# Performance work log

Measured on AMD Instinct MI355X. Metric: run time of the kernel, lower is better.

## Reference

```python
import jax, jax.numpy as jnp
import numpy as np

EPS = 1e-5
QSCALE = 2.0 ** 7  # input bitwidth 8 -> deterministic quantize round(x*2^(b-1))/2^(b-1)

@jax.custom_vjp
def ste_sign(x):
    # deterministic binarize: sign with sign(0)=+1; identity STE (matches .data trick in BinarizeLinear)
    return jnp.where(x >= 0, 1.0, -1.0).astype(x.dtype)

def _ss_fwd(x):
    return ste_sign(x), None

def _ss_bwd(_, g):
    return (g,)

ste_sign.defvjp(_ss_fwd, _ss_bwd)

@jax.custom_vjp
def binarize_act(x):
    # activation binarize: sign forward, clipped (hard-tanh) STE backward
    return jnp.where(x >= 0, 1.0, -1.0).astype(x.dtype)

def _ba_fwd(x):
    return binarize_act(x), x

def _ba_bwd(x, g):
    return (g * (jnp.abs(x) <= 1.0).astype(g.dtype),)

binarize_act.defvjp(_ba_fwd, _ba_bwd)

@jax.custom_vjp
def quantize8(x):
    return jnp.round(x * QSCALE) / QSCALE

def _q_fwd(x):
    return quantize8(x), None

def _q_bwd(_, g):
    return (g,)

quantize8.defvjp(_q_fwd, _q_bwd)

def blinear(x, W, b):
    # BinarizeLinear: binarize activations and weights, fp accumulate GEMM + bias
    return ste_sign(x) @ ste_sign(W).T + b

def bn_eval(x, g, be, m, v):
    return (x - m) * (g / jnp.sqrt(v + EPS)) + be

def setup_inputs() -> dict:
    key = jax.random.key(0)
    ks = jax.random.split(key, 16)
    B, D_IN, H, D_OUT = 8192, 4096, 4096, 1000
    d = {}
    d['x'] = jax.random.normal(ks[0], (B, D_IN), dtype=jnp.float32)
    dims = [(H, D_IN), (H, H), (D_OUT, H)]
    for i, (o, inp) in enumerate(dims, start=1):
        d[f'W{i}'] = jax.random.normal(ks[3 * i], (o, inp), dtype=jnp.float32) * (1.0 / np.sqrt(inp))
        d[f'b{i}'] = jnp.zeros((o,), dtype=jnp.float32)
        d[f'g{i}'] = jnp.ones((o,), dtype=jnp.float32)
        d[f'be{i}'] = jnp.zeros((o,), dtype=jnp.float32)
        d[f'm{i}'] = jax.random.normal(ks[3 * i + 1], (o,), dtype=jnp.float32) * 0.1
        d[f'v{i}'] = jax.random.uniform(ks[3 * i + 2], (o,), dtype=jnp.float32, minval=0.5, maxval=1.5)
    return d

def reference(x, W1, b1, g1, be1, m1, v1, W2, b2, g2, be2, m2, v2, W3, b3, g3, be3, m3, v3):
    h = quantize8(x)
    h = bn_eval(blinear(h, W1, b1), g1, be1, m1, v1)
    h = binarize_act(h)
    h = bn_eval(blinear(h, W2, b2), g2, be2, m2, v2)
    h = binarize_act(h)
    h = bn_eval(blinear(h, W3, b3), g3, be3, m3, v3)
    return h  # eval mode: no softmax
```

## Files before the change

kernel.cpp:

```cpp
#include <hip/hip_runtime.h>
#include <hip/hip_bf16.h>
#include <stdint.h>
#include <math.h>

typedef float  f32x4 __attribute__((ext_vector_type(4)));
typedef short  s16x8 __attribute__((ext_vector_type(8)));

#define BEPS 1e-5f

typedef const void __attribute__((address_space(1))) gvoid_t;
typedef void       __attribute__((address_space(3))) lvoid_t;

__device__ __forceinline__ void gload_lds16(const void* g, void* l) {
  __builtin_amdgcn_global_load_lds((gvoid_t*)g, (lvoid_t*)l, 16, 0, 0);
}

__global__ void k_sign(const float* __restrict__ in, ushort* __restrict__ out,
                       long n4, float thresh) {
  const long stride = (long)gridDim.x * blockDim.x;
  for (long i = (long)blockIdx.x * blockDim.x + threadIdx.x; i < n4; i += stride) {
    float4 v = reinterpret_cast<const float4*>(in)[i];
    ushort4 o;
    o.x = (v.x >= thresh) ? (ushort)0x3F80u : (ushort)0xBF80u;
    o.y = (v.y >= thresh) ? (ushort)0x3F80u : (ushort)0xBF80u;
    o.z = (v.z >= thresh) ? (ushort)0x3F80u : (ushort)0xBF80u;
    o.w = (v.w >= thresh) ? (ushort)0x3F80u : (ushort)0xBF80u;
    reinterpret_cast<ushort4*>(out)[i] = o;
  }
}

__global__ void k_sign_w3(const float* __restrict__ in, ushort* __restrict__ out) {
  const long n4 = 1024L * 1024;
  const long stride = (long)gridDim.x * blockDim.x;
  for (long i = (long)blockIdx.x * blockDim.x + threadIdx.x; i < n4; i += stride) {
    long row = i >> 10;
    ushort4 o;
    if (row < 1000) {
      float4 v = reinterpret_cast<const float4*>(in)[i];
      o.x = (v.x >= 0.f) ? (ushort)0x3F80u : (ushort)0xBF80u;
      o.y = (v.y >= 0.f) ? (ushort)0x3F80u : (ushort)0xBF80u;
      o.z = (v.z >= 0.f) ? (ushort)0x3F80u : (ushort)0xBF80u;
      o.w = (v.w >= 0.f) ? (ushort)0x3F80u : (ushort)0xBF80u;
    } else {
      o.x = o.y = o.z = o.w = (ushort)0x3F80u;
    }
    reinterpret_cast<ushort4*>(out)[i] = o;
  }
}

template<int EPI>
__global__ __launch_bounds__(256, 2)
void k_gemm_bt(const ushort* __restrict__ A,
               const ushort* __restrict__ B,
               void* __restrict__ Cout,
               const float* __restrict__ bias, const float* __restrict__ gam,
               const float* __restrict__ bet,  const float* __restrict__ mean,
               const float* __restrict__ var,
               int M, int Npad, int K, int Nreal, int ldC)
{
  __shared__ ushort As[128 * 32];
  __shared__ ushort Bs[128 * 32];

  const int tid  = threadIdx.x;
  const int lane = tid & 63;
  const int wave = tid >> 6;
  const int wr   = wave >> 1;
  const int wc   = wave & 1;
  const int fr   = lane & 15;
  const int fq   = lane >> 4;

  const int nwg = (int)gridDim.x;
  const int q   = nwg >> 3;
  const int bid = (int)blockIdx.x;
  const int swz = (bid & 7) * q + (bid >> 3);

  const int  nTN = Npad >> 7;
  const int  tm  = swz / nTN;
  const int  tn  = swz % nTN;
  const long m0  = (long)tm * 128;
  const long n0  = (long)tn * 128;

  f32x4 acc[4][4];
#pragma unroll
  for (int i = 0; i < 4; ++i)
#pragma unroll
    for (int j = 0; j < 4; ++j) acc[i][j] = (f32x4){0.f, 0.f, 0.f, 0.f};

  const int c0 = wave * 64 + lane;
  const int c1 = c0 + 256;
  const ushort* Ag0 = A + (m0 + (c0 >> 2)) * K + (c0 & 3) * 8;
  const ushort* Ag1 = A + (m0 + (c1 >> 2)) * K + (c1 & 3) * 8;
  const ushort* Bg0 = B + (n0 + (c0 >> 2)) * K + (c0 & 3) * 8;
  const ushort* Bg1 = B + (n0 + (c1 >> 2)) * K + (c1 & 3) * 8;
  ushort* AsP0 = As + c0 * 8;
  ushort* AsP1 = As + c1 * 8;
  ushort* BsP0 = Bs + c0 * 8;
  ushort* BsP1 = Bs + c1 * 8;

  const ushort* aRd = As + (wr * 64 + fr) * 32 + fq * 8;
  const ushort* bRd = Bs + (wc * 64 + fr) * 32 + fq * 8;

  const int KSTEPS = K >> 5;
  for (int ks = 0; ks < KSTEPS; ++ks) {
    gload_lds16(Ag0, AsP0);
    gload_lds16(Ag1, AsP1);
    gload_lds16(Bg0, BsP0);
    gload_lds16(Bg1, BsP1);
    Ag0 += 32; Ag1 += 32; Bg0 += 32; Bg1 += 32;
    __syncthreads();

    s16x8 aF[4], bF[4];
#pragma unroll
    for (int i = 0; i < 4; ++i) aF[i] = *(const s16x8*)(aRd + i * 16 * 32);
#pragma unroll
    for (int j = 0; j < 4; ++j) bF[j] = *(const s16x8*)(bRd + j * 16 * 32);
#pragma unroll
    for (int i = 0; i < 4; ++i)
#pragma unroll
      for (int j = 0; j < 4; ++j)
        acc[i][j] = __builtin_amdgcn_mfma_f32_16x16x32_bf16(aF[i], bF[j], acc[i][j], 0, 0, 0);
    __syncthreads();
  }

  if (EPI == 0) {
    ushort* O = (ushort*)Cout;
#pragma unroll
    for (int j = 0; j < 4; ++j) {
      const long gn = n0 + wc * 64 + j * 16 + fr;
      const float bb  = bias[gn];
      const float mm  = mean[gn];
      const float be_ = bet[gn];
      const float s   = gam[gn] / sqrtf(var[gn] + BEPS);
#pragma unroll
      for (int i = 0; i < 4; ++i) {
#pragma unroll
        for (int r = 0; r < 4; ++r) {
          const long gm = m0 + wr * 64 + i * 16 + fq * 4 + r;
          float h = (acc[i][j][r] + bb - mm) * s + be_;
          O[gm * (long)ldC + gn] = (h >= 0.f) ? (ushort)0x3F80u : (ushort)0xBF80u;
        }
      }
    }
  } else {
    float* O = (float*)Cout;
#pragma unroll
    for (int j = 0; j < 4; ++j) {
      const long gn = n0 + wc * 64 + j * 16 + fr;
      if (gn < Nreal) {
        const float bb  = bias[gn];
        const float mm  = mean[gn];
        const float be_ = bet[gn];
        const float s   = gam[gn] / sqrtf(var[gn] + BEPS);
#pragma unroll
        for (int i = 0; i < 4; ++i) {
#pragma unroll
          for (int r = 0; r < 4; ++r) {
            const long gm = m0 + wr * 64 + i * 16 + fq * 4 + r;
            float h = (acc[i][j][r] + bb - mm) * s + be_;
            O[gm * (long)ldC + gn] = h;
          }
        }
      }
    }
  }
}

extern "C" void kernel_launch(void* const* d_in, const int* in_sizes, int n_in,
                              void* d_out, int out_size, void* d_ws, size_t ws_size,
                              hipStream_t stream) {
  const float* x   = (const float*)d_in[0];
  const float* W1  = (const float*)d_in[1];
  const float* b1  = (const float*)d_in[2];
  const float* g1  = (const float*)d_in[3];
  const float* be1 = (const float*)d_in[4];
  const float* m1  = (const float*)d_in[5];
  const float* v1  = (const float*)d_in[6];
  const float* W2  = (const float*)d_in[7];
  const float* b2  = (const float*)d_in[8];
  const float* g2  = (const float*)d_in[9];
  const float* be2 = (const float*)d_in[10];
  const float* m2  = (const float*)d_in[11];
  const float* v2  = (const float*)d_in[12];
  const float* W3  = (const float*)d_in[13];
  const float* b3  = (const float*)d_in[14];
  const float* g3  = (const float*)d_in[15];
  const float* be3 = (const float*)d_in[16];
  const float* m3  = (const float*)d_in[17];
  const float* v3  = (const float*)d_in[18];
  float* out = (float*)d_out;

  char* ws = (char*)d_ws;
  ushort* ActA = (ushort*)ws;
  ushort* ActB = (ushort*)(ws + 67108864L);
  ushort* Wbuf = (ushort*)(ws + 2L * 67108864L);

  const long n4_x = 8192L * 4096 / 4;
  const long n4_w = 4096L * 4096 / 4;

  k_sign<<<2048, 256, 0, stream>>>(x, ActA, n4_x, -0.00390625f);
  k_sign<<<2048, 256, 0, stream>>>(W1, Wbuf, n4_w, 0.0f);
  k_gemm_bt<0><<<64 * 32, 256, 0, stream>>>(ActA, Wbuf, ActB, b1, g1, be1, m1, v1,
                                            8192, 4096, 4096, 4096, 4096);
  k_sign<<<2048, 256, 0, stream>>>(W2, Wbuf, n4_w, 0.0f);
  k_gemm_bt<0><<<64 * 32, 256, 0, stream>>>(ActB, Wbuf, ActA, b2, g2, be2, m2, v2,
                                            8192, 4096, 4096, 4096, 4096);
  k_sign_w3<<<1024, 256, 0, stream>>>(W3, Wbuf);
  k_gemm_bt<1><<<64 * 8, 256, 0, stream>>>(ActA, Wbuf, out, b3, g3, be3, m3, v3,
                                           8192, 1024, 4096, 1000, 1000);
}
```

Before: 1.033 ms.

## Replace 128x128 GEMM with pipelined 256x256 tile kernel for hidden layers

Adds a 512-thread GEMM kernel with 256x256 output tiles, K-step of 64, and double-buffered 128KB LDS. Global-to-LDS loads are interleaved between MFMA phases, and the LDS layout uses an XOR swizzle to avoid bank conflicts. It also raises wave priority around the MFMA blocks. The two 4096x4096 layers switch to this kernel, aiming to cut load stalls, barrier overhead and global traffic per FLOP. In exchange it uses more registers and LDS per block, which can limit occupancy, and the hand-written wait counts must be exactly right to avoid races.

```diff
diff --git a/kernel.cpp b/kernel.cpp
--- a/kernel.cpp
+++ b/kernel.cpp
@@ -48,10 +48,198 @@
   }
 }
 
+#define MF(a, b, c) __builtin_amdgcn_mfma_f32_16x16x32_bf16(a, b, c, 0, 0, 0)
+#define PH_MFMA(i0, i1) \
+  acc[i0][0]=MF(x0,b0k0,acc[i0][0]); acc[i0][0]=MF(x1,b0k1,acc[i0][0]); \
+  acc[i0][1]=MF(x0,b1k0,acc[i0][1]); acc[i0][1]=MF(x1,b1k1,acc[i0][1]); \
+  acc[i0][2]=MF(x0,b2k0,acc[i0][2]); acc[i0][2]=MF(x1,b2k1,acc[i0][2]); \
+  acc[i0][3]=MF(x0,b3k0,acc[i0][3]); acc[i0][3]=MF(x1,b3k1,acc[i0][3]); \
+  acc[i1][0]=MF(y0,b0k0,acc[i1][0]); acc[i1][0]=MF(y1,b0k1,acc[i1][0]); \
+  acc[i1][1]=MF(y0,b1k0,acc[i1][1]); acc[i1][1]=MF(y1,b1k1,acc[i1][1]); \
+  acc[i1][2]=MF(y0,b2k0,acc[i1][2]); acc[i1][2]=MF(y1,b2k1,acc[i1][2]); \
+  acc[i1][3]=MF(y0,b3k0,acc[i1][3]); acc[i1][3]=MF(y1,b3k1,acc[i1][3]);
+
+#define STG_A0(ko, bo) do { gload_lds16(Ag00 + (ko), &lds[(bo) + dst0]); \
+                            gload_lds16(Ag01 + (ko), &lds[(bo) + dst1]); } while (0)
+#define STG_A1(ko, bo) do { gload_lds16(Ag10 + (ko), &lds[(bo) + 8192 + dst0]); \
+                            gload_lds16(Ag11 + (ko), &lds[(bo) + 8192 + dst1]); } while (0)
+#define STG_B0(ko, bo) do { gload_lds16(Bg00 + (ko), &lds[(bo) + 16384 + dst0]); \
+                            gload_lds16(Bg01 + (ko), &lds[(bo) + 16384 + dst1]); } while (0)
+#define STG_B1(ko, bo) do { gload_lds16(Bg10 + (ko), &lds[(bo) + 24576 + dst0]); \
+                            gload_lds16(Bg11 + (ko), &lds[(bo) + 24576 + dst1]); } while (0)
+
+#define RA(bo, i, k) (*(const s16x8*)&lds[(bo) + aBase + (i) * 1024 + (k)])
+#define RB(bo, j, k) (*(const s16x8*)&lds[(bo) + bBase + (j) * 1024 + (k)])
+
+__global__ __launch_bounds__(512, 2)
+void k_gemm256(const ushort* __restrict__ A,
+               const ushort* __restrict__ B,
+               ushort* __restrict__ Cout,
+               const float* __restrict__ bias, const float* __restrict__ gam,
+               const float* __restrict__ bet,  const float* __restrict__ mean,
+               const float* __restrict__ var,
+               int M, int Npad, int K)
+{
+  extern __shared__ ushort lds[];
+
+  const int tid  = threadIdx.x;
+  const int lane = tid & 63;
+  const int wave = tid >> 6;
+  const int wr   = wave >> 2;
+  const int wc   = wave & 3;
+  const int fr   = lane & 15;
+  const int fq   = lane >> 4;
+
+  const int nwg = (int)gridDim.x;
+  const int q8  = nwg >> 3;
+  const int bid = (int)blockIdx.x;
+  const int swzb = (bid & 7) * q8 + (bid >> 3);
+  const int nTN = Npad >> 8;
+  const long m0 = (long)(swzb / nTN) * 256;
+  const long n0 = (long)(swzb % nTN) * 256;
+
+  const int colS = ((tid & 7) * 8) ^ (((tid >> 3) & 7) << 3);
+  const int r0   = tid >> 3;
+  const int dst0 = tid * 8;
+  const int dst1 = (tid + 512) * 8;
+  const ushort* Ag00 = A + (m0 +       r0     ) * (long)K + colS;
+  const ushort* Ag01 = A + (m0 +       r0 + 64) * (long)K + colS;
+  const ushort* Ag10 = A + (m0 + 128 + r0     ) * (long)K + colS;
+  const ushort* Ag11 = A + (m0 + 128 + r0 + 64) * (long)K + colS;
+  const ushort* Bg00 = B + (n0 +       r0     ) * (long)K + colS;
+  const ushort* Bg01 = B + (n0 +       r0 + 64) * (long)K + colS;
+  const ushort* Bg10 = B + (n0 + 128 + r0     ) * (long)K + colS;
+  const ushort* Bg11 = B + (n0 + 128 + r0 + 64) * (long)K + colS;
+
+  const int ce0   = (fq * 8) ^ ((fr & 7) << 3);
+  const int ce1   = ce0 ^ 32;
+  const int aBase = wr * 8192 + fr * 64;
+  const int bBase = 16384 + (wc >> 1) * 8192 + (wc & 1) * 4096 + fr * 64;
+
+  f32x4 acc[8][4];
+#pragma unroll
+  for (int i = 0; i < 8; ++i)
+#pragma unroll
+    for (int j = 0; j < 4; ++j) acc[i][j] = (f32x4){0.f, 0.f, 0.f, 0.f};
+
+  STG_A0(0, 0);      STG_A1(0, 0);      STG_B0(0, 0);      STG_B1(0, 0);
+  STG_A0(64, 32768); STG_A1(64, 32768); STG_B0(64, 32768); STG_B1(64, 32768);
+
+  const int NK = K >> 6;
+  for (int kt = 0; kt < NK - 2; ++kt) {
+    const int curO = (kt & 1) << 15;
+    const int nxtO = curO ^ 32768;
+    const int koA  = (kt + 1) << 6;
+    const int koB  = (kt + 2) << 6;
+
+    asm volatile("s_waitcnt vmcnt(4)" ::: "memory");
+    __builtin_amdgcn_s_barrier();
+    __builtin_amdgcn_sched_barrier(0);
+    s16x8 b0k0 = RB(curO,0,ce0), b0k1 = RB(curO,0,ce1),
+          b1k0 = RB(curO,1,ce0), b1k1 = RB(curO,1,ce1),
+          b2k0 = RB(curO,2,ce0), b2k1 = RB(curO,2,ce1),
+          b3k0 = RB(curO,3,ce0), b3k1 = RB(curO,3,ce1);
+    s16x8 x0 = RA(curO,0,ce0), x1 = RA(curO,0,ce1),
+          y0 = RA(curO,1,ce0), y1 = RA(curO,1,ce1);
+    if (kt >= 1) STG_A0(koA, nxtO);
+    asm volatile("s_waitcnt lgkmcnt(0)" ::: "memory");
+    __builtin_amdgcn_sched_barrier(0);
+    __builtin_amdgcn_s_setprio(1);
+    PH_MFMA(0, 1)
+    __builtin_amdgcn_s_setprio(0);
+    __builtin_amdgcn_s_barrier();
+
+    x0 = RA(curO,2,ce0); x1 = RA(curO,2,ce1);
+    y0 = RA(curO,3,ce0); y1 = RA(curO,3,ce1);
+    if (kt >= 1) STG_A1(koA, nxtO);
+    STG_B0(koB, curO);
+    asm volatile("s_waitcnt lgkmcnt(0)" ::: "memory");
+    __builtin_amdgcn_sched_barrier(0);
+    __builtin_amdgcn_s_setprio(1);
+    PH_MFMA(2, 3)
+    __builtin_amdgcn_s_setprio(0);
+    __builtin_amdgcn_s_barrier();
+
+    x0 = RA(curO,4,ce0); x1 = RA(curO,4,ce1);
+    y0 = RA(curO,5,ce0); y1 = RA(curO,5,ce1);
+    STG_B1(koB, curO);
+    asm volatile("s_waitcnt lgkmcnt(0)" ::: "memory");
+    __builtin_amdgcn_sched_barrier(0);
+    __builtin_amdgcn_s_setprio(1);
+    PH_MFMA(4, 5)
+    __builtin_amdgcn_s_setprio(0);
+    __builtin_amdgcn_s_barrier();
+
+    x0 = RA(curO,6,ce0); x1 = RA(curO,6,ce1);
+    y0 = RA(curO,7,ce0); y1 = RA(curO,7,ce1);
+    asm volatile("s_waitcnt lgkmcnt(0)" ::: "memory");
+    __builtin_amdgcn_sched_barrier(0);
+    __builtin_amdgcn_s_setprio(1);
+    PH_MFMA(6, 7)
+    __builtin_amdgcn_s_setprio(0);
+    __builtin_amdgcn_s_barrier();
+  }
+
+  {
+    const int lastO  = ((NK - 1) & 1) << 15;
+    const int koLast = (NK - 1) << 6;
+    STG_A0(koLast, lastO);
+    STG_A1(koLast, lastO);
+  }
+
+  asm volatile("s_waitcnt vmcnt(0)" ::: "memory");
+  __builtin_amdgcn_s_barrier();
+  __builtin_amdgcn_sched_barrier(0);
+  for (int kt = NK - 2; kt < NK; ++kt) {
+    const int curO = (kt & 1) << 15;
+    s16x8 b0k0 = RB(curO,0,ce0), b0k1 = RB(curO,0,ce1),
+          b1k0 = RB(curO,1,ce0), b1k1 = RB(curO,1,ce1),
+          b2k0 = RB(curO,2,ce0), b2k1 = RB(curO,2,ce1),
+          b3k0 = RB(curO,3,ce0), b3k1 = RB(curO,3,ce1);
+    s16x8 x0 = RA(curO,0,ce0), x1 = RA(curO,0,ce1),
+          y0 = RA(curO,1,ce0), y1 = RA(curO,1,ce1);
+    asm volatile("s_waitcnt lgkmcnt(0)" ::: "memory");
+    __builtin_amdgcn_sched_barrier(0);
+    PH_MFMA(0, 1)
+    x0 = RA(curO,2,ce0); x1 = RA(curO,2,ce1);
+    y0 = RA(curO,3,ce0); y1 = RA(curO,3,ce1);
+    asm volatile("s_waitcnt lgkmcnt(0)" ::: "memory");
+    __builtin_amdgcn_sched_barrier(0);
+    PH_MFMA(2, 3)
+    x0 = RA(curO,4,ce0); x1 = RA(curO,4,ce1);
+    y0 = RA(curO,5,ce0); y1 = RA(curO,5,ce1);
+    asm volatile("s_waitcnt lgkmcnt(0)" ::: "memory");
+    __builtin_amdgcn_sched_barrier(0);
+    PH_MFMA(4, 5)
+    x0 = RA(curO,6,ce0); x1 = RA(curO,6,ce1);
+    y0 = RA(curO,7,ce0); y1 = RA(curO,7,ce1);
+    asm volatile("s_waitcnt lgkmcnt(0)" ::: "memory");
+    __builtin_amdgcn_sched_barrier(0);
+    PH_MFMA(6, 7)
+  }
+
+#pragma unroll
+  for (int j = 0; j < 4; ++j) {
+    const long gn = n0 + wc * 64 + j * 16 + fr;
+    const float bb  = bias[gn];
+    const float mm  = mean[gn];
+    const float be_ = bet[gn];
+    const float s   = gam[gn] / sqrtf(var[gn] + BEPS);
+#pragma unroll
+    for (int i = 0; i < 8; ++i) {
+#pragma unroll
+      for (int rr = 0; rr < 4; ++rr) {
+        const long gm = m0 + wr * 128 + i * 16 + fq * 4 + rr;
+        float h = (acc[i][j][rr] + bb - mm) * s + be_;
+        Cout[gm * (long)Npad + gn] = (h >= 0.f) ? (ushort)0x3F80u : (ushort)0xBF80u;
+      }
+    }
+  }
+}
+
 template<int EPI>
 __global__ __launch_bounds__(256, 2)
-void k_gemm_bt(const ushort* __restrict__ A,
-               const ushort* __restrict__ B,
+void k_gemm_bt(const ushort* __restrict__ A, const ushort* __restrict__ B,
                void* __restrict__ Cout,
                const float* __restrict__ bias, const float* __restrict__ gam,
                const float* __restrict__ bet,  const float* __restrict__ mean,
@@ -199,11 +387,11 @@
 
   k_sign<<<2048, 256, 0, stream>>>(x, ActA, n4_x, -0.00390625f);
   k_sign<<<2048, 256, 0, stream>>>(W1, Wbuf, n4_w, 0.0f);
-  k_gemm_bt<0><<<64 * 32, 256, 0, stream>>>(ActA, Wbuf, ActB, b1, g1, be1, m1, v1,
-                                            8192, 4096, 4096, 4096, 4096);
+  k_gemm256<<<512, 512, 131072, stream>>>(ActA, Wbuf, ActB, b1, g1, be1, m1, v1,
+                                          8192, 4096, 4096);
   k_sign<<<2048, 256, 0, stream>>>(W2, Wbuf, n4_w, 0.0f);
-  k_gemm_bt<0><<<64 * 32, 256, 0, stream>>>(ActB, Wbuf, ActA, b2, g2, be2, m2, v2,
-                                            8192, 4096, 4096, 4096, 4096);
+  k_gemm256<<<512, 512, 131072, stream>>>(ActB, Wbuf, ActA, b2, g2, be2, m2, v2,
+                                          8192, 4096, 4096);
   k_sign_w3<<<1024, 256, 0, stream>>>(W3, Wbuf);
   k_gemm_bt<1><<<64 * 8, 256, 0, stream>>>(ActA, Wbuf, out, b3, g3, be3, m3, v3,
                                            8192, 1024, 4096, 1000, 1000);
```

New measurement: 839.3 us. -18.8%, faster.
